# Kernel tuning notes

Hardware: AMD Instinct MI355X
Metric: run time of the kernel (lower is better)

## Reference

```python
import jax, jax.numpy as jnp
import numpy as np

B, N, M12, H, O, I, DIFF = 8192, 100, 12, 64, 128, 12, 1.0
TWO_PI = 2.0 * np.pi


def _moments_single(xi, K):
    # xi: [N, 2] single sample; K: [12, 2] exponent pairs -> [12]
    xc = xi - xi.mean(axis=0)                 # center per-sample (mean over points)
    p = xc[:, None, :] ** K[None, :, :]       # [N, 12, 2]
    return jnp.sum(p[..., 0] * p[..., 1], axis=0)  # [12]


def setup_inputs() -> dict:
    key = jax.random.key(0)
    ks = jax.random.split(key, 8)
    # 12 integer central-moment exponent pairs (p, q)
    P = jnp.array([1, 2, 0, 2, 1, 3, 0, 2, 3, 1, 4, 0], jnp.float32)
    Q = jnp.array([1, 0, 2, 1, 2, 0, 3, 2, 1, 3, 0, 4], jnp.float32)
    K = jnp.stack([P, Q], axis=-1)            # [12, 2]

    x = jax.random.normal(ks[0], (B, N, 2), jnp.float32)
    t = jax.random.uniform(ks[1], (1,), jnp.float32, 0.1, 1.0)  # positive time
    W_fourier = jax.random.normal(ks[2], (H // 2,), jnp.float32) * 30.0

    def lin(k, fin, fout):
        bound = 1.0 / np.sqrt(fin)
        kw, kb = jax.random.split(k)
        W = jax.random.uniform(kw, (fin, fout), jnp.float32, -bound, bound)
        b = jax.random.uniform(kb, (fout,), jnp.float32, -bound, bound)
        return W, b

    embed_W, embed_b = lin(ks[3], H, H)
    lin1_W, lin1_b = lin(ks[4], I, H)
    lin2a_W, lin2a_b = lin(ks[5], H, O)
    lin2b_W, lin2b_b = lin(ks[6], O, I)
    lin2c_W, lin2c_b = lin(ks[7], I, I)
    return {
        'x': x, 't': t, 'K': K, 'W_fourier': W_fourier,
        'embed_W': embed_W, 'embed_b': embed_b,
        'lin1_W': lin1_W, 'lin1_b': lin1_b,
        'lin2a_W': lin2a_W, 'lin2a_b': lin2a_b,
        'lin2b_W': lin2b_W, 'lin2b_b': lin2b_b,
        'lin2c_W': lin2c_W, 'lin2c_b': lin2c_b,
    }


def reference(x, t, K, W_fourier, embed_W, embed_b, lin1_W, lin1_b,
              lin2a_W, lin2a_b, lin2b_W, lin2b_b, lin2c_W, lin2c_b):
    # Invariance encoding ('Moment' mode): [B, 12]
    m = jax.vmap(_moments_single, in_axes=(0, None))(x, K)
    h = jax.nn.gelu(m @ lin1_W + lin1_b, approximate=False)   # [B, H] (dropout = eval identity)
    # Gaussian Fourier time embedding: [1, H]
    xp = t[:, None] * W_fourier[None, :] * TWO_PI
    emb = jnp.concatenate([jnp.sin(xp), jnp.cos(xp)], axis=-1) @ embed_W + embed_b
    h = jax.nn.gelu((h + emb) @ lin2a_W + lin2a_b, approximate=False)
    h = jax.nn.gelu(h @ lin2b_W + lin2b_b, approximate=False)
    h = (h @ lin2c_W + lin2c_b) / jnp.sqrt(DIFF * t)          # [B, 12]
    # Per-sample jacobian of the moment map: [B, 12, N, 2]
    # (equals the block diagonal of torch.autograd.functional.jacobian over the batch)
    jac = jax.vmap(jax.jacrev(_moments_single), in_axes=(0, None))(x, K)
    # Replaces the (i, j) double loop of tiny matmuls with one batched contraction
    return jnp.einsum('bk,bknj->bnj', h, jac)                 # [B, N, 2]
```

## Files before the change

### kernel.cpp

```cpp
#include <hip/hip_runtime.h>
#include <hip/hip_bf16.h>


static __device__ __forceinline__ float gelu_f(float x) {
    float y = 0.7071067811865475f * x;
    float s = fabsf(y);
    float t = __builtin_amdgcn_rcpf(fmaf(0.3275911f, s, 1.0f));
    float p = t * fmaf(t, fmaf(t, fmaf(t, fmaf(t, 1.061405429f,
                    -1.453152027f), 1.421413741f), -0.284496736f), 0.254829592f);
    float e = __expf(-y * y);
    float ea = fmaf(-p, e, 1.0f);
    float erfv = copysignf(ea, y);
    return 0.5f * x * (1.0f + erfv);
}

#define DPP_ADD(v, ctrl) \
    v += __int_as_float(__builtin_amdgcn_update_dpp(0, __float_as_int(v), ctrl, 0xf, 0xf, true))

static __device__ __forceinline__ float wave_sum(float v) {
    DPP_ADD(v, 0x111);
    DPP_ADD(v, 0x112);
    DPP_ADD(v, 0x114);
    DPP_ADD(v, 0x118);
    DPP_ADD(v, 0x142);
    DPP_ADD(v, 0x143);
    return __int_as_float(__builtin_amdgcn_readlane(__float_as_int(v), 63));
}

#define TWO_PI_F 6.283185307179586f

__global__ __launch_bounds__(256) void scorenet_fused(
    const float* __restrict__ x,
    const float* __restrict__ t_in,
    const float* __restrict__ Wf,
    const float* __restrict__ embW,
    const float* __restrict__ embB,
    const float* __restrict__ W1,
    const float* __restrict__ b1,
    const float* __restrict__ W2a,
    const float* __restrict__ b2a,
    const float* __restrict__ W2b,
    const float* __restrict__ b2b,
    const float* __restrict__ W2c,
    const float* __restrict__ b2c,
    float* __restrict__ out,
    int B)
{
    __shared__ float s_f[64];
    __shared__ float s_emb[64];

    const int tid = threadIdx.x;
    const float tval = t_in[0];

    if (tid < 32) {
        float xp = tval * Wf[tid] * TWO_PI_F;
        s_f[tid]      = sinf(xp);
        s_f[tid + 32] = cosf(xp);
    }
    __syncthreads();
    if (tid < 64) {
        float acc = embB[tid];
        const float4* f4 = reinterpret_cast<const float4*>(s_f);
        #pragma unroll
        for (int c = 0; c < 16; ++c) {
            float4 a4 = f4[c];
            int j = 4 * c;
            acc = fmaf(a4.x, embW[(j+0)*64 + tid],
                  fmaf(a4.y, embW[(j+1)*64 + tid],
                  fmaf(a4.z, embW[(j+2)*64 + tid],
                  fmaf(a4.w, embW[(j+3)*64 + tid], acc))));
        }
        s_emb[tid] = acc;
    }
    __syncthreads();

    const int lane = tid & 63;
    const int b = blockIdx.x * 4 + (tid >> 6);
    if (b >= B) return;

    const float2* px = reinterpret_cast<const float2*>(x) + (size_t)b * 100;
    const bool has2 = lane < 36;

    float2 p0 = px[lane];
    float2 p1 = px[has2 ? lane + 64 : lane];
    float xa = p0.x, ya = p0.y;
    float xb = has2 ? p1.x : 0.0f;
    float yb = has2 ? p1.y : 0.0f;

    const float mux = wave_sum(xa + xb) * 0.01f;
    const float muy = wave_sum(ya + yb) * 0.01f;

    float ua = xa - mux, va = ya - muy;
    float ub = has2 ? (xb - mux) : 0.0f;
    float vb = has2 ? (yb - muy) : 0.0f;

    float ms[12];
    {
        float u2 = ua * ua, v2 = va * va;
        ms[0] = ua * va;   ms[1] = u2;        ms[2] = v2;
        ms[3] = u2 * va;   ms[4] = ua * v2;
        ms[5] = u2 * ua;   ms[6] = v2 * va;
        ms[7] = u2 * v2;   ms[8] = ms[5] * va; ms[9] = ua * ms[6];
        ms[10] = u2 * u2;  ms[11] = v2 * v2;
        float w2 = ub * ub, z2 = vb * vb;
        ms[0] += ub * vb;  ms[1] += w2;       ms[2] += z2;
        ms[3] += w2 * vb;  ms[4] += ub * z2;
        ms[5] += w2 * ub;  ms[6] += z2 * vb;
        ms[7] += w2 * z2;  ms[8] += w2 * ub * vb; ms[9] += ub * z2 * vb;
        ms[10] += w2 * w2; ms[11] += z2 * z2;
    }
    float m[12];
    #pragma unroll
    for (int k = 0; k < 12; ++k) m[k] = wave_sum(ms[k]);

    float a1 = b1[lane];
    #pragma unroll
    for (int k = 0; k < 12; ++k) a1 = fmaf(m[k], W1[k * 64 + lane], a1);
    float aval = gelu_f(a1) + s_emb[lane];

    float acc0 = b2a[lane];
    float acc1 = b2a[lane + 64];
    #pragma unroll
    for (int j = 0; j < 64; ++j) {
        float aj = __int_as_float(__builtin_amdgcn_readlane(__float_as_int(aval), j));
        acc0 = fmaf(aj, W2a[j * 128 + lane], acc0);
        acc1 = fmaf(aj, W2a[j * 128 + 64 + lane], acc1);
    }
    float h2lo = gelu_f(acc0), h2hi = gelu_f(acc1);

    float h3[12];
    #pragma unroll
    for (int k = 0; k < 12; ++k) {
        float p3 = fmaf(h2lo, W2b[lane * 12 + k], h2hi * W2b[(lane + 64) * 12 + k]);
        h3[k] = gelu_f(wave_sum(p3) + b2b[k]);
    }

    const float rst = rsqrtf(tval);
    float h[12];
    #pragma unroll
    for (int k = 0; k < 12; ++k) {
        float acc = b2c[k];
        #pragma unroll
        for (int j = 0; j < 12; ++j) acc = fmaf(h3[j], W2c[j * 12 + k], acc);
        h[k] = acc * rst;
    }

    const float inv_n = 0.01f;
    float c0 = (2.0f*h[3]*m[0] + h[4]*m[2] + 3.0f*h[5]*m[1] + 2.0f*h[7]*m[4]
              + 3.0f*h[8]*m[3] + h[9]*m[6] + 4.0f*h[10]*m[5]) * inv_n;
    float c1 = (h[3]*m[1] + 2.0f*h[4]*m[0] + 3.0f*h[6]*m[2] + 2.0f*h[7]*m[3]
              + h[8]*m[5] + 3.0f*h[9]*m[4] + 4.0f*h[11]*m[6]) * inv_n;

    const float A1 = 2.0f*h[1], A2 = h[0],      A3 = 3.0f*h[5], A4 = 2.0f*h[3], A5 = h[4];
    const float A6 = 4.0f*h[10],A7 = 3.0f*h[8], A8 = 2.0f*h[7], A9 = h[9];
    const float B1 = h[0],      B2 = 2.0f*h[2], B3 = h[3],      B4 = 2.0f*h[4], B5 = 3.0f*h[6];
    const float B6 = h[8],      B7 = 2.0f*h[7], B8 = 3.0f*h[9], B9 = 4.0f*h[11];

    float2* pout = reinterpret_cast<float2*>(out) + (size_t)b * 100;
    {
        float u = ua, v = va;
        float u2 = u*u, v2 = v*v;
        float o0 = A1*u + A2*v + A3*u2 + A4*u*v + A5*v2 + A6*u2*u + A7*u2*v + A8*u*v2 + A9*v2*v - c0;
        float o1 = B1*u + B2*v + B3*u2 + B4*u*v + B5*v2 + B6*u2*u + B7*u2*v + B8*u*v2 + B9*v2*v - c1;
        float2 r; r.x = o0; r.y = o1;
        pout[lane] = r;
    }
    if (has2) {
        float u = ub, v = vb;
        float u2 = u*u, v2 = v*v;
        float o0 = A1*u + A2*v + A3*u2 + A4*u*v + A5*v2 + A6*u2*u + A7*u2*v + A8*u*v2 + A9*v2*v - c0;
        float o1 = B1*u + B2*v + B3*u2 + B4*u*v + B5*v2 + B6*u2*u + B7*u2*v + B8*u*v2 + B9*v2*v - c1;
        float2 r; r.x = o0; r.y = o1;
        pout[lane + 64] = r;
    }
}

extern "C" void kernel_launch(void* const* d_in, const int* in_sizes, int n_in,
                              void* d_out, int out_size, void* d_ws, size_t ws_size,
                              hipStream_t stream) {
    const float* x    = (const float*)d_in[0];
    const float* t    = (const float*)d_in[1];
    const float* Wf   = (const float*)d_in[3];
    const float* embW = (const float*)d_in[4];
    const float* embB = (const float*)d_in[5];
    const float* W1   = (const float*)d_in[6];
    const float* b1   = (const float*)d_in[7];
    const float* W2a  = (const float*)d_in[8];
    const float* b2a  = (const float*)d_in[9];
    const float* W2b  = (const float*)d_in[10];
    const float* b2b  = (const float*)d_in[11];
    const float* W2c  = (const float*)d_in[12];
    const float* b2c  = (const float*)d_in[13];

    const int B = in_sizes[0] / 200;
    const int blocks = (B + 3) / 4;

    scorenet_fused<<<blocks, 256, 0, stream>>>(
        x, t, Wf, embW, embB, W1, b1, W2a, b2a, W2b, b2b, W2c, b2c,
        (float*)d_out, B);
}
```

Measured before the change: 103.2 us.

## Vectorize W2a/W2b weight loads with interleaved output mapping and occupancy hint

Each lane now owns outputs 2*lane and 2*lane+1 of the 128-wide layer, so W2a rows are read as float2 and W2b rows as six float4 loads prefetched early into registers. The 64-step FMA chain is split into two interleaved accumulators to shorten the dependency chain. The launch bounds also request 4 blocks per CU. The aim is fewer, wider global/L1 loads and more ILP, at the cost of 24 extra registers per thread under a tighter register cap.

```diff
diff --git a/kernel.cpp b/kernel.cpp
--- a/kernel.cpp
+++ b/kernel.cpp
@@ -29,7 +29,7 @@
 
 #define TWO_PI_F 6.283185307179586f
 
-__global__ __launch_bounds__(256) void scorenet_fused(
+__global__ __launch_bounds__(256, 4) void scorenet_fused(
     const float* __restrict__ x,
     const float* __restrict__ t_in,
     const float* __restrict__ Wf,
@@ -83,6 +83,17 @@
 
     float2 p0 = px[lane];
     float2 p1 = px[has2 ? lane + 64 : lane];
+
+    float wb[24];
+    {
+        const float4* w2b4 = reinterpret_cast<const float4*>(W2b + lane * 24);
+        #pragma unroll
+        for (int c = 0; c < 6; ++c) {
+            float4 q = w2b4[c];
+            wb[4*c+0] = q.x; wb[4*c+1] = q.y; wb[4*c+2] = q.z; wb[4*c+3] = q.w;
+        }
+    }
+
     float xa = p0.x, ya = p0.y;
     float xb = has2 ? p1.x : 0.0f;
     float yb = has2 ? p1.y : 0.0f;
@@ -118,20 +129,27 @@
     for (int k = 0; k < 12; ++k) a1 = fmaf(m[k], W1[k * 64 + lane], a1);
     float aval = gelu_f(a1) + s_emb[lane];
 
-    float acc0 = b2a[lane];
-    float acc1 = b2a[lane + 64];
-    #pragma unroll
-    for (int j = 0; j < 64; ++j) {
-        float aj = __int_as_float(__builtin_amdgcn_readlane(__float_as_int(aval), j));
-        acc0 = fmaf(aj, W2a[j * 128 + lane], acc0);
-        acc1 = fmaf(aj, W2a[j * 128 + 64 + lane], acc1);
-    }
-    float h2lo = gelu_f(acc0), h2hi = gelu_f(acc1);
+    const float2* w2a2 = reinterpret_cast<const float2*>(W2a);
+    float accE0 = b2a[2 * lane], accO0 = b2a[2 * lane + 1];
+    float accE1 = 0.0f, accO1 = 0.0f;
+    #pragma unroll
+    for (int j = 0; j < 64; j += 2) {
+        float aj0 = __int_as_float(__builtin_amdgcn_readlane(__float_as_int(aval), j));
+        float aj1 = __int_as_float(__builtin_amdgcn_readlane(__float_as_int(aval), j + 1));
+        float2 w0 = w2a2[(size_t)j * 64 + lane];
+        float2 w1v = w2a2[(size_t)(j + 1) * 64 + lane];
+        accE0 = fmaf(aj0, w0.x, accE0);
+        accO0 = fmaf(aj0, w0.y, accO0);
+        accE1 = fmaf(aj1, w1v.x, accE1);
+        accO1 = fmaf(aj1, w1v.y, accO1);
+    }
+    float h2e = gelu_f(accE0 + accE1);
+    float h2o = gelu_f(accO0 + accO1);
 
     float h3[12];
     #pragma unroll
     for (int k = 0; k < 12; ++k) {
-        float p3 = fmaf(h2lo, W2b[lane * 12 + k], h2hi * W2b[(lane + 64) * 12 + k]);
+        float p3 = fmaf(h2e, wb[k], h2o * wb[12 + k]);
         h3[k] = gelu_f(wave_sum(p3) + b2b[k]);
     }
 
```

After: 104.2 us. No clear change (+1.0%).

## Split into prep kernel with bf16-packed weights and two samples per wave

Applied to the files above, without the earlier changes.

Adds a single-block prep kernel that packs W2a and W2b into bf16 pairs and precomputes the time embedding once into workspace, so the main kernel no longer recomputes the embedding in every block. The main kernel processes two samples per wave, so each packed W2a load and weight register setup is shared by both samples. The W2c stage is distributed across lanes and broadcast with readlane. It keeps per-lane weights in registers under a min-occupancy launch bound. Rounding the weights to bf16 lowers precision, and the extra launch adds overhead.

```diff
diff --git a/kernel.cpp b/kernel.cpp
--- a/kernel.cpp
+++ b/kernel.cpp
@@ -1,6 +1,8 @@
 #include <hip/hip_runtime.h>
 #include <hip/hip_bf16.h>
 
+
+#define TWO_PI_F 6.283185307179586f
 
 static __device__ __forceinline__ float gelu_f(float x) {
     float y = 0.7071067811865475f * x;
@@ -10,8 +12,7 @@
                     -1.453152027f), 1.421413741f), -0.284496736f), 0.254829592f);
     float e = __expf(-y * y);
     float ea = fmaf(-p, e, 1.0f);
-    float erfv = copysignf(ea, y);
-    return 0.5f * x * (1.0f + erfv);
+    return 0.5f * x * (1.0f + copysignf(ea, y));
 }
 
 #define DPP_ADD(v, ctrl) \
@@ -27,31 +28,43 @@
     return __int_as_float(__builtin_amdgcn_readlane(__float_as_int(v), 63));
 }
 
-#define TWO_PI_F 6.283185307179586f
-
-__global__ __launch_bounds__(256) void scorenet_fused(
-    const float* __restrict__ x,
+static __device__ __forceinline__ float bcast_lane(float v, int l) {
+    return __int_as_float(__builtin_amdgcn_readlane(__float_as_int(v), l));
+}
+
+static __device__ __forceinline__ unsigned int f2bf(float f) {
+    unsigned int u = __float_as_uint(f);
+    return (u + 0x7fffu + ((u >> 16) & 1u)) >> 16;
+}
+
+__global__ __launch_bounds__(256) void scorenet_prep(
+    const float* __restrict__ W2a,
+    const float* __restrict__ W2b,
     const float* __restrict__ t_in,
     const float* __restrict__ Wf,
     const float* __restrict__ embW,
     const float* __restrict__ embB,
-    const float* __restrict__ W1,
-    const float* __restrict__ b1,
-    const float* __restrict__ W2a,
-    const float* __restrict__ b2a,
-    const float* __restrict__ W2b,
-    const float* __restrict__ b2b,
-    const float* __restrict__ W2c,
-    const float* __restrict__ b2c,
-    float* __restrict__ out,
-    int B)
+    unsigned int* __restrict__ wsA,
+    unsigned int* __restrict__ wsB,
+    float* __restrict__ wsE)
 {
     __shared__ float s_f[64];
-    __shared__ float s_emb[64];
-
     const int tid = threadIdx.x;
+
+    #pragma unroll
+    for (int i = tid; i < 4096; i += 256) {
+        int j = i >> 6, l = i & 63;
+        unsigned int lo = f2bf(W2a[j * 128 + 2 * l]);
+        unsigned int hi = f2bf(W2a[j * 128 + 2 * l + 1]);
+        wsA[i] = lo | (hi << 16);
+    }
+    #pragma unroll
+    for (int i = tid; i < 768; i += 256) {
+        unsigned int lo = f2bf(W2b[2 * i]);
+        unsigned int hi = f2bf(W2b[2 * i + 1]);
+        wsB[i] = lo | (hi << 16);
+    }
     const float tval = t_in[0];
-
     if (tid < 32) {
         float xp = tval * Wf[tid] * TWO_PI_F;
         s_f[tid]      = sinf(xp);
@@ -60,118 +73,173 @@
     __syncthreads();
     if (tid < 64) {
         float acc = embB[tid];
-        const float4* f4 = reinterpret_cast<const float4*>(s_f);
-        #pragma unroll
-        for (int c = 0; c < 16; ++c) {
-            float4 a4 = f4[c];
-            int j = 4 * c;
-            acc = fmaf(a4.x, embW[(j+0)*64 + tid],
-                  fmaf(a4.y, embW[(j+1)*64 + tid],
-                  fmaf(a4.z, embW[(j+2)*64 + tid],
-                  fmaf(a4.w, embW[(j+3)*64 + tid], acc))));
+        #pragma unroll 8
+        for (int j = 0; j < 64; ++j) acc = fmaf(s_f[j], embW[j * 64 + tid], acc);
+        wsE[tid] = acc;
+    }
+}
+
+__global__ __launch_bounds__(256, 4) void scorenet_main(
+    const float* __restrict__ x,
+    const float* __restrict__ t_in,
+    const float* __restrict__ W1,
+    const float* __restrict__ b1,
+    const float* __restrict__ b2a,
+    const float* __restrict__ b2b,
+    const float* __restrict__ W2c,
+    const float* __restrict__ b2c,
+    const unsigned int* __restrict__ wsA,
+    const unsigned int* __restrict__ wsB,
+    const float* __restrict__ wsE,
+    float* __restrict__ out,
+    int B)
+{
+    const int tid = threadIdx.x;
+    const int lane = tid & 63;
+    const int wv = tid >> 6;
+    const bool has2 = lane < 36;
+    const int b0 = (blockIdx.x * 4 + wv) * 2;
+    if (b0 >= B) return;
+
+    const float tval = t_in[0];
+    const float rst = rsqrtf(tval);
+    const float embv = wsE[lane];
+
+    float w1c[12];
+    #pragma unroll
+    for (int k = 0; k < 12; ++k) w1c[k] = W1[k * 64 + lane];
+    float wb[24];
+    #pragma unroll
+    for (int c = 0; c < 12; ++c) {
+        unsigned int u = wsB[lane * 12 + c];
+        wb[2 * c]     = __uint_as_float(u << 16);
+        wb[2 * c + 1] = __uint_as_float(u & 0xffff0000u);
+    }
+    const float b1v  = b1[lane];
+    const float b2aE = b2a[2 * lane], b2aO = b2a[2 * lane + 1];
+    const int kk = lane < 12 ? lane : 0;
+    float w2ck[12];
+    #pragma unroll
+    for (int j = 0; j < 12; ++j) w2ck[j] = W2c[j * 12 + kk];
+    const float b2ck = b2c[kk];
+    float b2bv[12];
+    #pragma unroll
+    for (int k = 0; k < 12; ++k) b2bv[k] = b2b[k];
+
+    const int bA = b0;
+    const int bBi = (b0 + 1 < B) ? b0 + 1 : B - 1;
+    const float2* pxA = reinterpret_cast<const float2*>(x) + (size_t)bA * 100;
+    const float2* pxB = reinterpret_cast<const float2*>(x) + (size_t)bBi * 100;
+    float2 PA0 = pxA[lane], PA1 = pxA[has2 ? lane + 64 : lane];
+    float2 PB0 = pxB[lane], PB1 = pxB[has2 ? lane + 64 : lane];
+
+    float aval[2], m[2][12];
+    float uas[2], vas[2], ubs[2], vbs[2];
+    #pragma unroll
+    for (int s = 0; s < 2; ++s) {
+        float xa = s ? PB0.x : PA0.x, ya = s ? PB0.y : PA0.y;
+        float xb = has2 ? (s ? PB1.x : PA1.x) : 0.0f;
+        float yb = has2 ? (s ? PB1.y : PA1.y) : 0.0f;
+
+        const float mux = wave_sum(xa + xb) * 0.01f;
+        const float muy = wave_sum(ya + yb) * 0.01f;
+
+        float ua = xa - mux, va = ya - muy;
+        float ub = has2 ? (xb - mux) : 0.0f;
+        float vb = has2 ? (yb - muy) : 0.0f;
+        uas[s] = ua; vas[s] = va; ubs[s] = ub; vbs[s] = vb;
+
+        float ms[12];
+        {
+            float u2 = ua * ua, v2 = va * va;
+            ms[0] = ua * va;   ms[1] = u2;         ms[2] = v2;
+            ms[3] = u2 * va;   ms[4] = ua * v2;
+            ms[5] = u2 * ua;   ms[6] = v2 * va;
+            ms[7] = u2 * v2;   ms[8] = ms[5] * va; ms[9] = ua * ms[6];
+            ms[10] = u2 * u2;  ms[11] = v2 * v2;
+            float w2 = ub * ub, z2 = vb * vb;
+            ms[0] += ub * vb;  ms[1] += w2;        ms[2] += z2;
+            ms[3] += w2 * vb;  ms[4] += ub * z2;
+            ms[5] += w2 * ub;  ms[6] += z2 * vb;
+            ms[7] += w2 * z2;  ms[8] += w2 * ub * vb; ms[9] += ub * z2 * vb;
+            ms[10] += w2 * w2; ms[11] += z2 * z2;
         }
-        s_emb[tid] = acc;
-    }
-    __syncthreads();
-
-    const int lane = tid & 63;
-    const int b = blockIdx.x * 4 + (tid >> 6);
-    if (b >= B) return;
-
-    const float2* px = reinterpret_cast<const float2*>(x) + (size_t)b * 100;
-    const bool has2 = lane < 36;
-
-    float2 p0 = px[lane];
-    float2 p1 = px[has2 ? lane + 64 : lane];
-    float xa = p0.x, ya = p0.y;
-    float xb = has2 ? p1.x : 0.0f;
-    float yb = has2 ? p1.y : 0.0f;
-
-    const float mux = wave_sum(xa + xb) * 0.01f;
-    const float muy = wave_sum(ya + yb) * 0.01f;
-
-    float ua = xa - mux, va = ya - muy;
-    float ub = has2 ? (xb - mux) : 0.0f;
-    float vb = has2 ? (yb - muy) : 0.0f;
-
-    float ms[12];
-    {
-        float u2 = ua * ua, v2 = va * va;
-        ms[0] = ua * va;   ms[1] = u2;        ms[2] = v2;
-        ms[3] = u2 * va;   ms[4] = ua * v2;
-        ms[5] = u2 * ua;   ms[6] = v2 * va;
-        ms[7] = u2 * v2;   ms[8] = ms[5] * va; ms[9] = ua * ms[6];
-        ms[10] = u2 * u2;  ms[11] = v2 * v2;
-        float w2 = ub * ub, z2 = vb * vb;
-        ms[0] += ub * vb;  ms[1] += w2;       ms[2] += z2;
-        ms[3] += w2 * vb;  ms[4] += ub * z2;
-        ms[5] += w2 * ub;  ms[6] += z2 * vb;
-        ms[7] += w2 * z2;  ms[8] += w2 * ub * vb; ms[9] += ub * z2 * vb;
-        ms[10] += w2 * w2; ms[11] += z2 * z2;
-    }
-    float m[12];
-    #pragma unroll
-    for (int k = 0; k < 12; ++k) m[k] = wave_sum(ms[k]);
-
-    float a1 = b1[lane];
-    #pragma unroll
-    for (int k = 0; k < 12; ++k) a1 = fmaf(m[k], W1[k * 64 + lane], a1);
-    float aval = gelu_f(a1) + s_emb[lane];
-
-    float acc0 = b2a[lane];
-    float acc1 = b2a[lane + 64];
+        #pragma unroll
+        for (int k = 0; k < 12; ++k) m[s][k] = wave_sum(ms[k]);
+
+        float a1 = b1v;
+        #pragma unroll
+        for (int k = 0; k < 12; ++k) a1 = fmaf(m[s][k], w1c[k], a1);
+        aval[s] = gelu_f(a1) + embv;
+    }
+
+    float aE0 = b2aE, aO0 = b2aO, aE1 = b2aE, aO1 = b2aO;
     #pragma unroll
     for (int j = 0; j < 64; ++j) {
-        float aj = __int_as_float(__builtin_amdgcn_readlane(__float_as_int(aval), j));
-        acc0 = fmaf(aj, W2a[j * 128 + lane], acc0);
-        acc1 = fmaf(aj, W2a[j * 128 + 64 + lane], acc1);
-    }
-    float h2lo = gelu_f(acc0), h2hi = gelu_f(acc1);
-
-    float h3[12];
-    #pragma unroll
-    for (int k = 0; k < 12; ++k) {
-        float p3 = fmaf(h2lo, W2b[lane * 12 + k], h2hi * W2b[(lane + 64) * 12 + k]);
-        h3[k] = gelu_f(wave_sum(p3) + b2b[k]);
-    }
-
-    const float rst = rsqrtf(tval);
-    float h[12];
-    #pragma unroll
-    for (int k = 0; k < 12; ++k) {
-        float acc = b2c[k];
-        #pragma unroll
-        for (int j = 0; j < 12; ++j) acc = fmaf(h3[j], W2c[j * 12 + k], acc);
-        h[k] = acc * rst;
-    }
-
-    const float inv_n = 0.01f;
-    float c0 = (2.0f*h[3]*m[0] + h[4]*m[2] + 3.0f*h[5]*m[1] + 2.0f*h[7]*m[4]
-              + 3.0f*h[8]*m[3] + h[9]*m[6] + 4.0f*h[10]*m[5]) * inv_n;
-    float c1 = (h[3]*m[1] + 2.0f*h[4]*m[0] + 3.0f*h[6]*m[2] + 2.0f*h[7]*m[3]
-              + h[8]*m[5] + 3.0f*h[9]*m[4] + 4.0f*h[11]*m[6]) * inv_n;
-
-    const float A1 = 2.0f*h[1], A2 = h[0],      A3 = 3.0f*h[5], A4 = 2.0f*h[3], A5 = h[4];
-    const float A6 = 4.0f*h[10],A7 = 3.0f*h[8], A8 = 2.0f*h[7], A9 = h[9];
-    const float B1 = h[0],      B2 = 2.0f*h[2], B3 = h[3],      B4 = 2.0f*h[4], B5 = 3.0f*h[6];
-    const float B6 = h[8],      B7 = 2.0f*h[7], B8 = 3.0f*h[9], B9 = 4.0f*h[11];
-
-    float2* pout = reinterpret_cast<float2*>(out) + (size_t)b * 100;
-    {
-        float u = ua, v = va;
-        float u2 = u*u, v2 = v*v;
-        float o0 = A1*u + A2*v + A3*u2 + A4*u*v + A5*v2 + A6*u2*u + A7*u2*v + A8*u*v2 + A9*v2*v - c0;
-        float o1 = B1*u + B2*v + B3*u2 + B4*u*v + B5*v2 + B6*u2*u + B7*u2*v + B8*u*v2 + B9*v2*v - c1;
-        float2 r; r.x = o0; r.y = o1;
-        pout[lane] = r;
-    }
-    if (has2) {
-        float u = ub, v = vb;
-        float u2 = u*u, v2 = v*v;
-        float o0 = A1*u + A2*v + A3*u2 + A4*u*v + A5*v2 + A6*u2*u + A7*u2*v + A8*u*v2 + A9*v2*v - c0;
-        float o1 = B1*u + B2*v + B3*u2 + B4*u*v + B5*v2 + B6*u2*u + B7*u2*v + B8*u*v2 + B9*v2*v - c1;
-        float2 r; r.x = o0; r.y = o1;
-        pout[lane + 64] = r;
+        unsigned int w = wsA[j * 64 + lane];
+        float we = __uint_as_float(w << 16);
+        float wo = __uint_as_float(w & 0xffff0000u);
+        float aj0 = bcast_lane(aval[0], j);
+        float aj1 = bcast_lane(aval[1], j);
+        aE0 = fmaf(aj0, we, aE0);
+        aO0 = fmaf(aj0, wo, aO0);
+        aE1 = fmaf(aj1, we, aE1);
+        aO1 = fmaf(aj1, wo, aO1);
+    }
+
+    #pragma unroll
+    for (int s = 0; s < 2; ++s) {
+        float h2e = gelu_f(s ? aE1 : aE0);
+        float h2o = gelu_f(s ? aO1 : aO0);
+
+        float h3[12];
+        #pragma unroll
+        for (int k = 0; k < 12; ++k) {
+            float p3 = fmaf(h2e, wb[k], h2o * wb[12 + k]);
+            h3[k] = gelu_f(wave_sum(p3) + b2bv[k]);
+        }
+
+        float acch = b2ck;
+        #pragma unroll
+        for (int j = 0; j < 12; ++j) acch = fmaf(h3[j], w2ck[j], acch);
+        acch *= rst;
+        float h[12];
+        #pragma unroll
+        for (int k = 0; k < 12; ++k) h[k] = bcast_lane(acch, k);
+
+        const float inv_n = 0.01f;
+        float c0 = (2.0f*h[3]*m[s][0] + h[4]*m[s][2] + 3.0f*h[5]*m[s][1]
+                  + 2.0f*h[7]*m[s][4] + 3.0f*h[8]*m[s][3] + h[9]*m[s][6]
+                  + 4.0f*h[10]*m[s][5]) * inv_n;
+        float c1 = (h[3]*m[s][1] + 2.0f*h[4]*m[s][0] + 3.0f*h[6]*m[s][2]
+                  + 2.0f*h[7]*m[s][3] + h[8]*m[s][5] + 3.0f*h[9]*m[s][4]
+                  + 4.0f*h[11]*m[s][6]) * inv_n;
+
+        const float A1 = 2.0f*h[1], A2 = h[0],      A3 = 3.0f*h[5], A4 = 2.0f*h[3], A5 = h[4];
+        const float A6 = 4.0f*h[10],A7 = 3.0f*h[8], A8 = 2.0f*h[7], A9 = h[9];
+        const float B1 = h[0],      B2 = 2.0f*h[2], B3 = h[3],      B4 = 2.0f*h[4], B5 = 3.0f*h[6];
+        const float B6 = h[8],      B7 = 2.0f*h[7], B8 = 3.0f*h[9], B9 = 4.0f*h[11];
+
+        const int b = b0 + s;
+        if (b < B) {
+            float2* pout = reinterpret_cast<float2*>(out) + (size_t)b * 100;
+            {
+                float u = uas[s], v = vas[s];
+                float u2 = u*u, v2 = v*v;
+                float o0 = A1*u + A2*v + A3*u2 + A4*u*v + A5*v2 + A6*u2*u + A7*u2*v + A8*u*v2 + A9*v2*v - c0;
+                float o1 = B1*u + B2*v + B3*u2 + B4*u*v + B5*v2 + B6*u2*u + B7*u2*v + B8*u*v2 + B9*v2*v - c1;
+                float2 r; r.x = o0; r.y = o1;
+                pout[lane] = r;
+            }
+            if (has2) {
+                float u = ubs[s], v = vbs[s];
+                float u2 = u*u, v2 = v*v;
+                float o0 = A1*u + A2*v + A3*u2 + A4*u*v + A5*v2 + A6*u2*u + A7*u2*v + A8*u*v2 + A9*v2*v - c0;
+                float o1 = B1*u + B2*v + B3*u2 + B4*u*v + B5*v2 + B6*u2*u + B7*u2*v + B8*u*v2 + B9*v2*v - c1;
+                float2 r; r.x = o0; r.y = o1;
+                pout[lane + 64] = r;
+            }
+        }
     }
 }
 
@@ -192,10 +260,15 @@
     const float* W2c  = (const float*)d_in[12];
     const float* b2c  = (const float*)d_in[13];
 
+    unsigned int* wsA = (unsigned int*)d_ws;
+    unsigned int* wsB = (unsigned int*)((char*)d_ws + 16384);
+    float*        wsE = (float*)((char*)d_ws + 16384 + 3072);
+
     const int B = in_sizes[0] / 200;
-    const int blocks = (B + 3) / 4;
-
-    scorenet_fused<<<blocks, 256, 0, stream>>>(
-        x, t, Wf, embW, embB, W1, b1, W2a, b2a, W2b, b2b, W2c, b2c,
+    const int blocks = (B + 7) / 8;
+
+    scorenet_prep<<<1, 256, 0, stream>>>(W2a, W2b, t, Wf, embW, embB, wsA, wsB, wsE);
+    scorenet_main<<<blocks, 256, 0, stream>>>(
+        x, t, W1, b1, b2a, b2b, W2c, b2c, wsA, wsB, wsE,
         (float*)d_out, B);
 }
```

New measurement: 138.3 us. 34.1% more time.

## Stage W2a/W2b as packed bf16 in LDS and lane-parallelize final layer

Applied to the files above, without the earlier changes.

Each block now converts W2a and W2b to bf16 pairs and stages them in shared memory, so the per-wave dense layers read from LDS instead of global memory. The W2a loop is restructured so each lane computes an even/odd output pair, with split accumulators. The x loads are issued before the weight staging to overlap latency, and the final 12x12 layer is computed one output per lane and then broadcast. This adds per-block staging cost and cuts the precision of two weight matrices to bf16, which may exceed tolerance.

```diff
diff --git a/kernel.cpp b/kernel.cpp
--- a/kernel.cpp
+++ b/kernel.cpp
@@ -1,6 +1,8 @@
 #include <hip/hip_runtime.h>
 #include <hip/hip_bf16.h>
 
+
+#define TWO_PI_F 6.283185307179586f
 
 static __device__ __forceinline__ float gelu_f(float x) {
     float y = 0.7071067811865475f * x;
@@ -10,8 +12,7 @@
                     -1.453152027f), 1.421413741f), -0.284496736f), 0.254829592f);
     float e = __expf(-y * y);
     float ea = fmaf(-p, e, 1.0f);
-    float erfv = copysignf(ea, y);
-    return 0.5f * x * (1.0f + erfv);
+    return 0.5f * x * (1.0f + copysignf(ea, y));
 }
 
 #define DPP_ADD(v, ctrl) \
@@ -27,9 +28,22 @@
     return __int_as_float(__builtin_amdgcn_readlane(__float_as_int(v), 63));
 }
 
-#define TWO_PI_F 6.283185307179586f
-
-__global__ __launch_bounds__(256) void scorenet_fused(
+static __device__ __forceinline__ float bcast_lane(float v, int l) {
+    return __int_as_float(__builtin_amdgcn_readlane(__float_as_int(v), l));
+}
+
+static __device__ __forceinline__ unsigned int f2bf(float f) {
+    unsigned int u = __float_as_uint(f);
+    return (u + 0x7fffu + ((u >> 16) & 1u)) >> 16;
+}
+static __device__ __forceinline__ float bf_lo(unsigned int u) {
+    return __uint_as_float(u << 16);
+}
+static __device__ __forceinline__ float bf_hi(unsigned int u) {
+    return __uint_as_float(u & 0xffff0000u);
+}
+
+__global__ __launch_bounds__(256, 4) void scorenet_fused(
     const float* __restrict__ x,
     const float* __restrict__ t_in,
     const float* __restrict__ Wf,
@@ -46,18 +60,40 @@
     float* __restrict__ out,
     int B)
 {
+    __shared__ unsigned int s_wa[4096];
+    __shared__ unsigned int s_wb[768];
     __shared__ float s_f[64];
     __shared__ float s_emb[64];
 
     const int tid = threadIdx.x;
+    const int lane = tid & 63;
+    const int wv = tid >> 6;
+    const bool has2 = lane < 36;
+    const int b = blockIdx.x * 4 + wv;
     const float tval = t_in[0];
 
-    if (tid < 32) {
-        float xp = tval * Wf[tid] * TWO_PI_F;
-        s_f[tid]      = sinf(xp);
-        s_f[tid + 32] = cosf(xp);
+    const int bc = (b < B) ? b : B - 1;
+    const float2* px = reinterpret_cast<const float2*>(x) + (size_t)bc * 100;
+    float2 p0 = px[lane];
+    float2 p1 = px[has2 ? lane + 64 : lane];
+
+    for (int i = tid; i < 4096; i += 256) {
+        int j = i >> 6, l = i & 63;
+        const float2 w = reinterpret_cast<const float2*>(W2a)[j * 64 + l];
+        s_wa[i] = f2bf(w.x) | (f2bf(w.y) << 16);
+    }
+    for (int i = tid; i < 768; i += 256) {
+        int c = i >> 6, l = i & 63;
+        s_wb[i] = f2bf(W2b[2 * l * 12 + c]) | (f2bf(W2b[(2 * l + 1) * 12 + c]) << 16);
+    }
+    if (tid >= 224) {
+        int i = tid - 224;
+        float xp = tval * Wf[i] * TWO_PI_F;
+        s_f[i]      = sinf(xp);
+        s_f[i + 32] = cosf(xp);
     }
     __syncthreads();
+
     if (tid < 64) {
         float acc = embB[tid];
         const float4* f4 = reinterpret_cast<const float4*>(s_f);
@@ -73,16 +109,10 @@
         s_emb[tid] = acc;
     }
     __syncthreads();
-
-    const int lane = tid & 63;
-    const int b = blockIdx.x * 4 + (tid >> 6);
     if (b >= B) return;
 
-    const float2* px = reinterpret_cast<const float2*>(x) + (size_t)b * 100;
-    const bool has2 = lane < 36;
-
-    float2 p0 = px[lane];
-    float2 p1 = px[has2 ? lane + 64 : lane];
+    const float rst = rsqrtf(tval);
+
     float xa = p0.x, ya = p0.y;
     float xb = has2 ? p1.x : 0.0f;
     float yb = has2 ? p1.y : 0.0f;
@@ -97,13 +127,13 @@
     float ms[12];
     {
         float u2 = ua * ua, v2 = va * va;
-        ms[0] = ua * va;   ms[1] = u2;        ms[2] = v2;
+        ms[0] = ua * va;   ms[1] = u2;         ms[2] = v2;
         ms[3] = u2 * va;   ms[4] = ua * v2;
         ms[5] = u2 * ua;   ms[6] = v2 * va;
         ms[7] = u2 * v2;   ms[8] = ms[5] * va; ms[9] = ua * ms[6];
         ms[10] = u2 * u2;  ms[11] = v2 * v2;
         float w2 = ub * ub, z2 = vb * vb;
-        ms[0] += ub * vb;  ms[1] += w2;       ms[2] += z2;
+        ms[0] += ub * vb;  ms[1] += w2;        ms[2] += z2;
         ms[3] += w2 * vb;  ms[4] += ub * z2;
         ms[5] += w2 * ub;  ms[6] += z2 * vb;
         ms[7] += w2 * z2;  ms[8] += w2 * ub * vb; ms[9] += ub * z2 * vb;
@@ -118,32 +148,38 @@
     for (int k = 0; k < 12; ++k) a1 = fmaf(m[k], W1[k * 64 + lane], a1);
     float aval = gelu_f(a1) + s_emb[lane];
 
-    float acc0 = b2a[lane];
-    float acc1 = b2a[lane + 64];
-    #pragma unroll
-    for (int j = 0; j < 64; ++j) {
-        float aj = __int_as_float(__builtin_amdgcn_readlane(__float_as_int(aval), j));
-        acc0 = fmaf(aj, W2a[j * 128 + lane], acc0);
-        acc1 = fmaf(aj, W2a[j * 128 + 64 + lane], acc1);
-    }
-    float h2lo = gelu_f(acc0), h2hi = gelu_f(acc1);
+    const float2 b2av = reinterpret_cast<const float2*>(b2a)[lane];
+    float aE0 = b2av.x, aO0 = b2av.y, aE1 = 0.0f, aO1 = 0.0f;
+    #pragma unroll
+    for (int j = 0; j < 64; j += 2) {
+        unsigned int u0 = s_wa[j * 64 + lane];
+        unsigned int u1 = s_wa[(j + 1) * 64 + lane];
+        float aj0 = bcast_lane(aval, j);
+        float aj1 = bcast_lane(aval, j + 1);
+        aE0 = fmaf(aj0, bf_lo(u0), aE0);
+        aO0 = fmaf(aj0, bf_hi(u0), aO0);
+        aE1 = fmaf(aj1, bf_lo(u1), aE1);
+        aO1 = fmaf(aj1, bf_hi(u1), aO1);
+    }
+    float h2e = gelu_f(aE0 + aE1);
+    float h2o = gelu_f(aO0 + aO1);
 
     float h3[12];
     #pragma unroll
     for (int k = 0; k < 12; ++k) {
-        float p3 = fmaf(h2lo, W2b[lane * 12 + k], h2hi * W2b[(lane + 64) * 12 + k]);
+        unsigned int u = s_wb[k * 64 + lane];
+        float p3 = fmaf(h2e, bf_lo(u), h2o * bf_hi(u));
         h3[k] = gelu_f(wave_sum(p3) + b2b[k]);
     }
 
-    const float rst = rsqrtf(tval);
+    const int kk = lane < 12 ? lane : 0;
+    float acch = b2c[kk];
+    #pragma unroll
+    for (int j = 0; j < 12; ++j) acch = fmaf(h3[j], W2c[j * 12 + kk], acch);
+    acch *= rst;
     float h[12];
     #pragma unroll
-    for (int k = 0; k < 12; ++k) {
-        float acc = b2c[k];
-        #pragma unroll
-        for (int j = 0; j < 12; ++j) acc = fmaf(h3[j], W2c[j * 12 + k], acc);
-        h[k] = acc * rst;
-    }
+    for (int k = 0; k < 12; ++k) h[k] = bcast_lane(acch, k);
 
     const float inv_n = 0.01f;
     float c0 = (2.0f*h[3]*m[0] + h[4]*m[2] + 3.0f*h[5]*m[1] + 2.0f*h[7]*m[4]
```

New measurement: 135.5 us. +31.3%, slower.
